# Kernel optimization log

Measured on AMD Instinct MI355X. Metric: run time of the kernel, lower is better.

Reference implementation:

```python
import jax, jax.numpy as jnp
import numpy as np

N = 100000      # nodes
E = 1600000     # edges
G = 100         # graphs in batch
D_IN, H, OUT = 3, 128, 10


def gcn_conv(x, W, b, src, dst, n_nodes):
    """PyG GCNConv with default add_self_loops=True, symmetric normalization.
    out_i = sum_{j->i} d_j^-1/2 d_i^-1/2 (x_j W) + d_i^-1 (x_i W) + b
    where d includes the self-loop (+1)."""
    h = x @ W                                                   # [N, F]
    ones = jnp.ones((src.shape[0],), dtype=x.dtype)
    deg = jax.ops.segment_sum(ones, dst, num_segments=n_nodes) + 1.0  # self-loop
    dinv_sqrt = jax.lax.rsqrt(deg)
    norm = dinv_sqrt[src] * dinv_sqrt[dst]                      # [E]
    msg = h[src] * norm[:, None]                                # gather + scale
    agg = jax.ops.segment_sum(msg, dst, num_segments=n_nodes)   # scatter-add
    out = agg + h * (1.0 / deg)[:, None] + b                    # self-loop term + bias
    return out


def setup_inputs() -> dict:
    key = jax.random.key(0)
    ks = jax.random.split(key, 9)
    x = jax.random.normal(ks[0], (N, D_IN), dtype=jnp.float32)
    edge_index = jax.random.randint(ks[1], (2, E), 0, N)
    batch = jnp.sort(jax.random.randint(ks[2], (N,), 0, G))
    W1 = jax.random.normal(ks[3], (D_IN, H), dtype=jnp.float32) * (1.0 / np.sqrt(D_IN))
    b1 = jnp.zeros((H,), dtype=jnp.float32)
    W2 = jax.random.normal(ks[4], (H, H), dtype=jnp.float32) * (1.0 / np.sqrt(H))
    b2 = jnp.zeros((H,), dtype=jnp.float32)
    Wl = jax.random.normal(ks[5], (H, OUT), dtype=jnp.float32) * (1.0 / np.sqrt(H))
    bl = jnp.zeros((OUT,), dtype=jnp.float32)
    return {"x": x, "edge_index": edge_index, "batch": batch,
            "W1": W1, "b1": b1, "W2": W2, "b2": b2, "Wl": Wl, "bl": bl}


def reference(x, edge_index, batch, W1, b1, W2, b2, Wl, bl):
    src, dst = edge_index[0], edge_index[1]
    h = jax.nn.relu(gcn_conv(x, W1, b1, src, dst, N))
    h = jax.nn.relu(gcn_conv(h, W2, b2, src, dst, N))
    # global mean pool over graphs
    sums = jax.ops.segment_sum(h, batch, num_segments=G)                 # [G, H]
    cnts = jax.ops.segment_sum(jnp.ones((N,), h.dtype), batch, num_segments=G)
    pooled = sums / jnp.maximum(cnts, 1.0)[:, None]
    # dropout p=0.5 is identity in eval mode
    return pooled @ Wl + bl                                              # [G, OUT]
```

## Files before the change

kernel.cpp:

```cpp
#include <hip/hip_runtime.h>


#define DIN 3
#define H 128
#define OUTF 10
#define NWEIGHT (384 + 128 + 16384 + 128 + 1280 + 10)
#define ECH 2048
#define RGSH 9
#define RGSIZE 512
#define W2FRAG_N 16384
#define CHE 512

typedef float gcn364_f2 __attribute__((ext_vector_type(2)));
typedef float gcn364_f4 __attribute__((ext_vector_type(4)));
typedef short gcn364_s8 __attribute__((ext_vector_type(8)));

__device__ __forceinline__ float gcn364_bf2f(unsigned short u) {
    return __uint_as_float(((unsigned int)u) << 16);
}
__device__ __forceinline__ unsigned short gcn364_f2bf(float f) {
    unsigned int u = __float_as_uint(f);
    u += 0x7FFFu + ((u >> 16) & 1u);
    return (unsigned short)(u >> 16);
}

__device__ __forceinline__ int gcn364_probe(const unsigned short* __restrict__ xs16) {
    int lane = threadIdx.x & 63;
    int outl = 0;
    #pragma unroll
    for (int k = 0; k < 4; k++) {
        unsigned short u = xs16[lane * 4 + k];
        int e = (u >> 7) & 0xFF;
        outl += (e < 100 || e > 140) ? 1 : 0;
    }
    #pragma unroll
    for (int d = 1; d < 64; d <<= 1) outl += __shfl_xor(outl, d);
    return (outl > 32) ? 1 : 0;
}

static __global__ void gcn364_histconv(const void* __restrict__ x,
                                       const void* __restrict__ W1, const void* __restrict__ b1,
                                       const void* __restrict__ W2, const void* __restrict__ b2,
                                       const void* __restrict__ Wl, const void* __restrict__ bl,
                                       int* __restrict__ flag,
                                       float4* __restrict__ xf4, float* __restrict__ wf,
                                       unsigned short* __restrict__ w2frag,
                                       float* __restrict__ pooled,
                                       const int* __restrict__ edst,
                                       int* __restrict__ hist,
                                       int N, int E, int S, int RG, int GH) {
    __shared__ int h[256];
    if (blockIdx.x < (unsigned)S) {
        h[threadIdx.x] = 0;
        __syncthreads();
        int elo = blockIdx.x * ECH;
        int ehi = elo + ECH; if (ehi > E) ehi = E;
        #pragma unroll 4
        for (int e = elo + threadIdx.x; e < ehi; e += 256)
            atomicAdd(&h[edst[e] >> RGSH], 1);
        __syncthreads();
        if (threadIdx.x < RG) hist[blockIdx.x * RG + threadIdx.x] = h[threadIdx.x];
    }
    int i = blockIdx.x * blockDim.x + threadIdx.x;
    if (i < GH) pooled[i] = 0.0f;
    int total = N + NWEIGHT;
    if ((int)blockIdx.x * 256 < total) {
        int fl = gcn364_probe((const unsigned short*)x);
        if (i == 0) *flag = fl;
        if (i < N) {
            float a, b, c;
            if (fl) {
                const float* xs = (const float*)x;
                a = xs[3 * i]; b = xs[3 * i + 1]; c = xs[3 * i + 2];
            } else {
                const unsigned short* xs = (const unsigned short*)x;
                a = gcn364_bf2f(xs[3 * i]);
                b = gcn364_bf2f(xs[3 * i + 1]);
                c = gcn364_bf2f(xs[3 * i + 2]);
            }
            xf4[i] = make_float4(a, b, c, 0.f);
        } else if (i < total) {
            int j = i - N;
            const void* srcp;
            if      (j < 384)                       { srcp = W1; }
            else if ((j -= 384)   < 128)            { srcp = b1; }
            else if ((j -= 128)   < 16384)          { srcp = W2; }
            else if ((j -= 16384) < 128)            { srcp = b2; }
            else if ((j -= 128)   < 1280)           { srcp = Wl; }
            else    { j -= 1280;                      srcp = bl; }
            wf[i - N] = fl ? ((const float*)srcp)[j]
                           : gcn364_bf2f(((const unsigned short*)srcp)[j]);
        }
        if (i < W2FRAG_N) {
            int fl2 = fl;
            int j = i & 7;
            int l = (i >> 3) & 63;
            int c = (i >> 9) & 3;
            int t = i >> 11;
            int k = c * 32 + (l >> 4) * 8 + j;
            int n = t * 16 + (l & 15);
            float w = fl2 ? ((const float*)W2)[k * H + n]
                          : gcn364_bf2f(((const unsigned short*)W2)[k * H + n]);
            w2frag[i] = gcn364_f2bf(w);
        }
    }
}

static __global__ void gcn364_scanHpar(int* __restrict__ hist,
                                       int* __restrict__ regionBase,
                                       int S, int RG) {
    __shared__ int sh[1024];
    int r = blockIdx.x;
    int t = threadIdx.x;
    int carry = 0;
    for (int s0 = 0; s0 < S; s0 += 1024) {
        int s = s0 + t;
        int c = (s < S) ? hist[s * RG + r] : 0;
        sh[t] = c;
        __syncthreads();
        for (int d = 1; d < 1024; d <<= 1) {
            int v = (t >= d) ? sh[t - d] : 0;
            __syncthreads();
            sh[t] += v;
            __syncthreads();
        }
        if (s < S) hist[s * RG + r] = carry + sh[t] - c;
        int tot = sh[1023];
        __syncthreads();
        carry += tot;
    }
    if (t == 0) regionBase[r] = carry;
}

static __global__ void gcn364_scanR(int* __restrict__ regionBase,
                                    int RG, int E) {
    __shared__ int sh[256];
    int t = threadIdx.x;
    int c = (t < RG) ? regionBase[t] : 0;
    sh[t] = c;
    __syncthreads();
    for (int d = 1; d < 256; d <<= 1) {
        int v = (t >= d) ? sh[t - d] : 0;
        __syncthreads();
        sh[t] += v;
        __syncthreads();
    }
    if (t < RG) regionBase[t] = sh[t] - c;
    if (t == 0) regionBase[RG] = E;
}

static __global__ void gcn364_partition(const int* __restrict__ src,
                                        const int* __restrict__ dst,
                                        const int* __restrict__ hist,
                                        const int* __restrict__ regionBase,
                                        int* __restrict__ epack,
                                        int E, int RG) {
    __shared__ int cur[256];
    int s = blockIdx.x;
    if (threadIdx.x < RG)
        cur[threadIdx.x] = hist[s * RG + threadIdx.x] + regionBase[threadIdx.x];
    __syncthreads();
    int elo = s * ECH;
    int ehi = elo + ECH; if (ehi > E) ehi = E;
    #pragma unroll 4
    for (int e = elo + threadIdx.x; e < ehi; e += 256) {
        int d = dst[e];
        int sv = src[e];
        int p = atomicAdd(&cur[d >> RGSH], 1);
        epack[p] = ((d & (RGSIZE - 1)) << 17) | sv;
    }
}

static __global__ void gcn364_build(const int* __restrict__ epack,
                                    const int* __restrict__ regionBase,
                                    int* __restrict__ off,
                                    int* __restrict__ esrc,
                                    float4* __restrict__ xf4,
                                    int N) {
    __shared__ int sdeg[RGSIZE];
    __shared__ int stmp[256];
    int r = blockIdx.x;
    int nlo = r << RGSH;
    int nn = N - nlo; if (nn > RGSIZE) nn = RGSIZE;
    int e0 = regionBase[r];
    int e1 = regionBase[r + 1];
    int t = threadIdx.x;
    int bdim = blockDim.x;

    if (t < RGSIZE) sdeg[t] = 0;
    __syncthreads();
    #pragma unroll 4
    for (int p = e0 + t; p < e1; p += bdim)
        atomicAdd(&sdeg[epack[p] >> 17], 1);
    __syncthreads();

    int a0 = 0, a1 = 0, psum = 0;
    if (t < 256) {
        a0 = sdeg[2 * t];
        a1 = sdeg[2 * t + 1];
        psum = a0 + a1;
        stmp[t] = psum;
    }
    __syncthreads();
    for (int d = 1; d < 256; d <<= 1) {
        int val = (t >= d && t < 256) ? stmp[t - d] : 0;
        __syncthreads();
        if (t < 256) stmp[t] += val;
        __syncthreads();
    }
    if (t < 256) {
        int excl = stmp[t] - psum;

        if (2 * t < nn)     off[nlo + 2 * t]     = e0 + excl + a0;
        if (2 * t + 1 < nn) off[nlo + 2 * t + 1] = e0 + excl + a0 + a1;
        if (2 * t < nn) {
            float di = rsqrtf((float)a0 + 1.0f);
            float4 xv = xf4[nlo + 2 * t];
            xv.x *= di; xv.y *= di; xv.z *= di; xv.w = di;
            xf4[nlo + 2 * t] = xv;
        }
        if (2 * t + 1 < nn) {
            float di = rsqrtf((float)a1 + 1.0f);
            float4 xv = xf4[nlo + 2 * t + 1];
            xv.x *= di; xv.y *= di; xv.z *= di; xv.w = di;
            xf4[nlo + 2 * t + 1] = xv;
        }
        sdeg[2 * t]     = e0 + excl;
        sdeg[2 * t + 1] = e0 + excl + a0;
    }
    __syncthreads();
    #pragma unroll 4
    for (int p = e0 + t; p < e1; p += bdim) {
        int v = epack[p];
        int q = atomicAdd(&sdeg[v >> 17], 1);
        esrc[q] = v & 0x1FFFF;
    }
}

static __global__ void gcn364_aggu(const int* __restrict__ esrc,
                                   const int* __restrict__ off,
                                   const float4* __restrict__ xf4,
                                   float4* __restrict__ u4, int N) {
    int lane = threadIdx.x & 63;
    int wv = threadIdx.x >> 6;
    int grp = lane >> 4;
    int sub = lane & 15;
    int i = (blockIdx.x * 4 + wv) * 4 + grp;

    float a0 = 0.f, a1 = 0.f, a2 = 0.f;
    if (i < N) {
        int p0 = (i == 0) ? 0 : off[i - 1];
        int p1 = off[i];
        for (int p = p0 + sub; p < p1; p += 16) {
            float4 sv = xf4[esrc[p]];
            a0 += sv.x; a1 += sv.y; a2 += sv.z;
        }
    }
    for (int d = 1; d < 16; d <<= 1) {
        a0 += __shfl_xor(a0, d);
        a1 += __shfl_xor(a1, d);
        a2 += __shfl_xor(a2, d);
    }
    if (i < N && sub == 0) {
        float4 xi = xf4[i];
        float di = xi.w;
        u4[i] = make_float4(di * (a0 + xi.x), di * (a1 + xi.y), di * (a2 + xi.z), di);
    }
}

__device__ __forceinline__ void gcn364_edge(const float4 u,
                                            const gcn364_f2* wa2, const gcn364_f2* wb2,
                                            const gcn364_f2* wc2, const gcn364_f2* bb2,
                                            gcn364_f2* acc) {
    gcn364_f2 ux = {u.x, u.x}, uy = {u.y, u.y}, uz = {u.z, u.z}, uw = {u.w, u.w};
    gcn364_f2 zero = {0.f, 0.f};
    #pragma unroll
    for (int q = 0; q < 4; q++) {
        gcn364_f2 t = ux * wa2[q] + uy * wb2[q] + uz * wc2[q] + bb2[q];
        t = __builtin_elementwise_max(t, zero);
        acc[q] += uw * t;
    }
}

#define MPB 16
static __global__ __launch_bounds__(256, 8) void gcn364_agg2pool(
        const int* __restrict__ esrc, const int* __restrict__ off,
        const float4* __restrict__ u4,
        const float* __restrict__ w1f, const float* __restrict__ b1f,
        const unsigned short* __restrict__ w2frag, const float* __restrict__ b2f,
        const int* __restrict__ batch, float* __restrict__ pooled, int N) {
    __shared__ unsigned short vshb[MPB][H + 8];
    __shared__ float4 sstage[CHE];
    __shared__ int soff[MPB + 1];
    __shared__ float spool[2][H];
    int i0 = blockIdx.x * MPB;
    int tid = threadIdx.x;
    int wave = tid >> 6;
    int lane = tid & 63;
    int grp = lane >> 4;
    int sub = lane & 15;
    int node = wave * 4 + grp;
    int i = i0 + node;

    if (tid <= MPB) {
        int idx = i0 - 1 + tid;
        int cidx = idx < N - 1 ? idx : N - 1;
        soff[tid] = (idx < 0) ? 0 : off[cidx];
    }

    gcn364_f2 wa2[4], wb2[4], wc2[4], bb2[4];
    #pragma unroll
    for (int q = 0; q < 4; q++) {
        int f = sub * 8 + q * 2;
        wa2[q] = (gcn364_f2){w1f[f], w1f[f + 1]};
        wb2[q] = (gcn364_f2){w1f[H + f], w1f[H + f + 1]};
        wc2[q] = (gcn364_f2){w1f[2 * H + f], w1f[2 * H + f + 1]};
        bb2[q] = (gcn364_f2){b1f[f], b1f[f + 1]};
    }
    __syncthreads();

    int s  = soff[node];
    int e  = soff[node + 1];
    int e0 = soff[0];
    int e1 = soff[MPB];

    gcn364_f2 acc[4];
    acc[0] = acc[1] = acc[2] = acc[3] = (gcn364_f2){0.f, 0.f};
    for (int cb = e0; cb < e1; cb += CHE) {
        int ce = cb + CHE; if (ce > e1) ce = e1;
        for (int p = cb + tid; p < ce; p += 256)
            sstage[p - cb] = u4[esrc[p]];
        __syncthreads();
        int lo = s > cb ? s : cb;
        int hi = e < ce ? e : ce;
        #pragma unroll 4
        for (int p = lo; p < hi; p++) {
            float4 u = sstage[p - cb];
            gcn364_edge(u, wa2, wb2, wc2, bb2, acc);
        }
        __syncthreads();
    }
    float di = 0.f;
    if (i < N) {
        float4 uS = u4[i];
        gcn364_edge(uS, wa2, wb2, wc2, bb2, acc);
        di = uS.w;
    }
    {
        gcn364_s8 o;
        o[0] = (short)gcn364_f2bf(acc[0].x * di);
        o[1] = (short)gcn364_f2bf(acc[0].y * di);
        o[2] = (short)gcn364_f2bf(acc[1].x * di);
        o[3] = (short)gcn364_f2bf(acc[1].y * di);
        o[4] = (short)gcn364_f2bf(acc[2].x * di);
        o[5] = (short)gcn364_f2bf(acc[2].y * di);
        o[6] = (short)gcn364_f2bf(acc[3].x * di);
        o[7] = (short)gcn364_f2bf(acc[3].y * di);
        *(gcn364_s8*)&vshb[node][sub * 8] = o;
    }
    __syncthreads();

    int m = lane & 15;
    int quad = lane >> 4;
    int g0 = batch[i0];
    gcn364_s8 af[4];
    #pragma unroll
    for (int c = 0; c < 4; c++)
        af[c] = *(const gcn364_s8*)&vshb[m][c * 32 + quad * 8];

    #pragma unroll
    for (int tt = 0; tt < 2; tt++) {
        int t = wave * 2 + tt;
        gcn364_f4 cacc = {0.f, 0.f, 0.f, 0.f};
        #pragma unroll
        for (int c = 0; c < 4; c++) {
            gcn364_s8 bf8 = *(const gcn364_s8*)&w2frag[(((t * 4 + c) * 64) + lane) * 8];
            cacc = __builtin_amdgcn_mfma_f32_16x16x32_bf16(af[c], bf8, cacc, 0, 0, 0);
        }
        int feat = t * 16 + m;
        float bb = b2f[feat];
        int baseRow = quad * 4;
        float sum0 = 0.0f, sum1 = 0.0f;
        #pragma unroll
        for (int r = 0; r < 4; r++) {
            int ii = i0 + baseRow + r;
            if (ii >= N) continue;
            float val = fmaxf(cacc[r] + bb, 0.0f);
            if (batch[ii] == g0) sum0 += val; else sum1 += val;
        }
        sum0 += __shfl_xor(sum0, 16); sum0 += __shfl_xor(sum0, 32);
        sum1 += __shfl_xor(sum1, 16); sum1 += __shfl_xor(sum1, 32);
        if (quad == 0) {
            spool[0][feat] = sum0;
            spool[1][feat] = sum1;
        }
    }
    __syncthreads();
    {
        int slot = tid >> 7;
        int f = tid & (H - 1);
        float v = spool[slot][f];
        if (v != 0.0f) {
            int il = i0 + MPB - 1; if (il > N - 1) il = N - 1;
            int g = slot ? batch[il] : g0;
            atomicAdd(&pooled[g * H + f], v);
        }
    }
}

static __global__ void gcn364_final(const float* __restrict__ pooled,
                                    const int* __restrict__ batch,
                                    const float* __restrict__ wlf,
                                    const float* __restrict__ blf,
                                    const int* __restrict__ flag,
                                    void* __restrict__ out, int N, int G) {
    int g = blockIdx.x;
    int o = threadIdx.x;
    if (g >= G || o >= OUTF) return;
    int lo = 0, hi = N;
    while (lo < hi) { int m = (lo + hi) >> 1; if (batch[m] < g) lo = m + 1; else hi = m; }
    int a = lo;
    lo = 0; hi = N;
    while (lo < hi) { int m = (lo + hi) >> 1; if (batch[m] < g + 1) lo = m + 1; else hi = m; }
    float cn = (float)(lo - a);
    float inv = 1.0f / fmaxf(cn, 1.0f);
    float acc = 0.0f;
    for (int k = 0; k < H; k++)
        acc += pooled[g * H + k] * wlf[k * OUTF + o];
    float v = acc * inv + blf[o];
    if (*flag) ((float*)out)[g * OUTF + o] = v;
    else       ((unsigned short*)out)[g * OUTF + o] = gcn364_f2bf(v);
}

extern "C" void kernel_launch(void* const* d_in, const int* in_sizes, int n_in,
                              void* d_out, int out_size, void* d_ws, size_t ws_size,
                              hipStream_t stream) {
    const void* x  = d_in[0];
    const int* edge_index = (const int*)d_in[1];
    const int* batch      = (const int*)d_in[2];
    const void* W1 = d_in[3];
    const void* b1 = d_in[4];
    const void* W2 = d_in[5];
    const void* b2 = d_in[6];
    const void* Wl = d_in[7];
    const void* bl = d_in[8];

    const int N = in_sizes[0] / DIN;
    const int E = in_sizes[1] / 2;
    const int G = out_size / OUTF;
    const int* src = edge_index;
    const int* dst = edge_index + E;
    const int SH = (E + 8191) / 8192;
    const int S  = (E + ECH - 1) / ECH;
    const int RG = (N + RGSIZE - 1) >> RGSH;
    const int GH = G * H;

    char* wsb = (char*)d_ws;
    float* pooled     = (float*)wsb;
    int*   histLeg    = (int*)(pooled + (size_t)GH);
    int*   regionBase = histLeg + (size_t)SH * RG;
    int*   off        = regionBase + RG + 1;
    int*   flag       = off + N;
    size_t ofs = (((size_t)((char*)(flag + 1) - wsb)) + 15) & ~(size_t)15;
    float4* xf4  = (float4*)(wsb + ofs);
    float4* u4   = xf4 + N;
    float*  wf   = (float*)(u4 + N);
    size_t ofs2 = (((size_t)((char*)(wf + NWEIGHT) - wsb)) + 15) & ~(size_t)15;
    unsigned short* w2frag = (unsigned short*)(wsb + ofs2);
    int*    epack = (int*)(w2frag + W2FRAG_N);
    int*    esrc  = epack + E;
    int*    hist  = esrc;

    float* w1f = wf;
    float* b1f = w1f + 384;
    float* b2f = b1f + 128 + 16384;
    float* wlf = b2f + 128;
    float* blf = wlf + 1280;

    {
        int convBlocks = (N + NWEIGHT + 255) / 256;
        int gmax = (S > convBlocks) ? S : convBlocks;
        gcn364_histconv<<<gmax, 256, 0, stream>>>(
            x, W1, b1, W2, b2, Wl, bl, flag, xf4, wf, w2frag, pooled,
            dst, hist, N, E, S, RG, GH);
    }
    gcn364_scanHpar<<<RG, 1024, 0, stream>>>(hist, regionBase, S, RG);
    gcn364_scanR<<<1, 256, 0, stream>>>(regionBase, RG, E);
    gcn364_partition<<<S, 256, 0, stream>>>(src, dst, hist, regionBase, epack, E, RG);
    gcn364_build<<<RG, 1024, 0, stream>>>(epack, regionBase, off, esrc, xf4, N);
    gcn364_aggu<<<(N + 15) / 16, 256, 0, stream>>>(esrc, off, xf4, u4, N);
    gcn364_agg2pool<<<(N + MPB - 1) / MPB, 256, 0, stream>>>(
        esrc, off, u4, w1f, b1f, w2frag, b2f, batch, pooled, N);
    gcn364_final<<<G, 64, 0, stream>>>(pooled, batch, wlf, blf, flag, d_out, N, G);
}
```

Measured before the change: 186.5 us.

## Map each wave across one node's features and process 64 nodes per block

The second aggregation kernel used to give each node a 16-lane group, with each lane handling 8 features. It now gives each node the full 64-lane wave, with each lane handling 2 features, and walks 4 nodes in sequence, so lanes no longer diverge when neighbouring nodes have different degrees. Each block now covers 64 nodes as four 16-node MFMA sub-tiles and adds the pooled sums into shared memory, which cuts the number of blocks and global atomics. The cost is a longer serial loop inside each block, extra barriers, and the existing assumption that a block's nodes span at most two graphs, now stretched over 64 nodes.

Measured after the change: 212.7 us. 1.14x slower.

```diff
diff --git a/kernel.cpp b/kernel.cpp
--- a/kernel.cpp
+++ b/kernel.cpp
@@ -268,28 +268,25 @@
     }
 }
 
-__device__ __forceinline__ void gcn364_edge(const float4 u,
-                                            const gcn364_f2* wa2, const gcn364_f2* wb2,
-                                            const gcn364_f2* wc2, const gcn364_f2* bb2,
-                                            gcn364_f2* acc) {
+__device__ __forceinline__ void gcn364_edge2(const float4 u,
+                                             const gcn364_f2 wa, const gcn364_f2 wb,
+                                             const gcn364_f2 wc, const gcn364_f2 bb,
+                                             gcn364_f2* acc) {
     gcn364_f2 ux = {u.x, u.x}, uy = {u.y, u.y}, uz = {u.z, u.z}, uw = {u.w, u.w};
     gcn364_f2 zero = {0.f, 0.f};
-    #pragma unroll
-    for (int q = 0; q < 4; q++) {
-        gcn364_f2 t = ux * wa2[q] + uy * wb2[q] + uz * wc2[q] + bb2[q];
-        t = __builtin_elementwise_max(t, zero);
-        acc[q] += uw * t;
-    }
-}
-
-#define MPB 16
+    gcn364_f2 t = ux * wa + uy * wb + uz * wc + bb;
+    t = __builtin_elementwise_max(t, zero);
+    *acc += uw * t;
+}
+
+#define MPB 64
 static __global__ __launch_bounds__(256, 8) void gcn364_agg2pool(
         const int* __restrict__ esrc, const int* __restrict__ off,
         const float4* __restrict__ u4,
         const float* __restrict__ w1f, const float* __restrict__ b1f,
         const unsigned short* __restrict__ w2frag, const float* __restrict__ b2f,
         const int* __restrict__ batch, float* __restrict__ pooled, int N) {
-    __shared__ unsigned short vshb[MPB][H + 8];
+    __shared__ unsigned short vshb[16][H + 8];
     __shared__ float4 sstage[CHE];
     __shared__ int soff[MPB + 1];
     __shared__ float spool[2][H];
@@ -297,105 +294,104 @@
     int tid = threadIdx.x;
     int wave = tid >> 6;
     int lane = tid & 63;
-    int grp = lane >> 4;
-    int sub = lane & 15;
-    int node = wave * 4 + grp;
-    int i = i0 + node;
 
     if (tid <= MPB) {
         int idx = i0 - 1 + tid;
         int cidx = idx < N - 1 ? idx : N - 1;
         soff[tid] = (idx < 0) ? 0 : off[cidx];
     }
-
-    gcn364_f2 wa2[4], wb2[4], wc2[4], bb2[4];
-    #pragma unroll
-    for (int q = 0; q < 4; q++) {
-        int f = sub * 8 + q * 2;
-        wa2[q] = (gcn364_f2){w1f[f], w1f[f + 1]};
-        wb2[q] = (gcn364_f2){w1f[H + f], w1f[H + f + 1]};
-        wc2[q] = (gcn364_f2){w1f[2 * H + f], w1f[2 * H + f + 1]};
-        bb2[q] = (gcn364_f2){b1f[f], b1f[f + 1]};
-    }
-    __syncthreads();
-
-    int s  = soff[node];
-    int e  = soff[node + 1];
-    int e0 = soff[0];
-    int e1 = soff[MPB];
-
-    gcn364_f2 acc[4];
-    acc[0] = acc[1] = acc[2] = acc[3] = (gcn364_f2){0.f, 0.f};
-    for (int cb = e0; cb < e1; cb += CHE) {
-        int ce = cb + CHE; if (ce > e1) ce = e1;
-        for (int p = cb + tid; p < ce; p += 256)
-            sstage[p - cb] = u4[esrc[p]];
-        __syncthreads();
-        int lo = s > cb ? s : cb;
-        int hi = e < ce ? e : ce;
-        #pragma unroll 4
-        for (int p = lo; p < hi; p++) {
-            float4 u = sstage[p - cb];
-            gcn364_edge(u, wa2, wb2, wc2, bb2, acc);
-        }
-        __syncthreads();
-    }
-    float di = 0.f;
-    if (i < N) {
-        float4 uS = u4[i];
-        gcn364_edge(uS, wa2, wb2, wc2, bb2, acc);
-        di = uS.w;
-    }
+    spool[tid >> 7][tid & (H - 1)] = 0.0f;
+
+    gcn364_f2 wa, wb, wc, bb;
     {
-        gcn364_s8 o;
-        o[0] = (short)gcn364_f2bf(acc[0].x * di);
-        o[1] = (short)gcn364_f2bf(acc[0].y * di);
-        o[2] = (short)gcn364_f2bf(acc[1].x * di);
-        o[3] = (short)gcn364_f2bf(acc[1].y * di);
-        o[4] = (short)gcn364_f2bf(acc[2].x * di);
-        o[5] = (short)gcn364_f2bf(acc[2].y * di);
-        o[6] = (short)gcn364_f2bf(acc[3].x * di);
-        o[7] = (short)gcn364_f2bf(acc[3].y * di);
-        *(gcn364_s8*)&vshb[node][sub * 8] = o;
-    }
-    __syncthreads();
-
-    int m = lane & 15;
-    int quad = lane >> 4;
+        int f = lane * 2;
+        wa = (gcn364_f2){w1f[f], w1f[f + 1]};
+        wb = (gcn364_f2){w1f[H + f], w1f[H + f + 1]};
+        wc = (gcn364_f2){w1f[2 * H + f], w1f[2 * H + f + 1]};
+        bb = (gcn364_f2){b1f[f], b1f[f + 1]};
+    }
     int g0 = batch[i0];
-    gcn364_s8 af[4];
-    #pragma unroll
-    for (int c = 0; c < 4; c++)
-        af[c] = *(const gcn364_s8*)&vshb[m][c * 32 + quad * 8];
-
-    #pragma unroll
-    for (int tt = 0; tt < 2; tt++) {
-        int t = wave * 2 + tt;
-        gcn364_f4 cacc = {0.f, 0.f, 0.f, 0.f};
+    __syncthreads();
+
+    for (int sub = 0; sub < 4; sub++) {
+        int nb = sub * 16;
+        int e0 = soff[nb];
+        int e1 = soff[nb + 16];
+
+        gcn364_f2 acc[4];
+        acc[0] = acc[1] = acc[2] = acc[3] = (gcn364_f2){0.f, 0.f};
+        for (int cb = e0; cb < e1; cb += CHE) {
+            int ce = cb + CHE; if (ce > e1) ce = e1;
+            for (int p = cb + tid; p < ce; p += 256)
+                sstage[p - cb] = u4[esrc[p]];
+            __syncthreads();
+            #pragma unroll
+            for (int nn = 0; nn < 4; nn++) {
+                int node = nb + wave * 4 + nn;
+                int lo = soff[node];     if (lo < cb) lo = cb;
+                int hi = soff[node + 1]; if (hi > ce) hi = ce;
+                #pragma unroll 4
+                for (int p = lo; p < hi; p++) {
+                    float4 u = sstage[p - cb];
+                    gcn364_edge2(u, wa, wb, wc, bb, &acc[nn]);
+                }
+            }
+            __syncthreads();
+        }
         #pragma unroll
-        for (int c = 0; c < 4; c++) {
-            gcn364_s8 bf8 = *(const gcn364_s8*)&w2frag[(((t * 4 + c) * 64) + lane) * 8];
-            cacc = __builtin_amdgcn_mfma_f32_16x16x32_bf16(af[c], bf8, cacc, 0, 0, 0);
-        }
-        int feat = t * 16 + m;
-        float bb = b2f[feat];
-        int baseRow = quad * 4;
-        float sum0 = 0.0f, sum1 = 0.0f;
+        for (int nn = 0; nn < 4; nn++) {
+            int nodeL = wave * 4 + nn;
+            int i = i0 + nb + nodeL;
+            float di = 0.f;
+            if (i < N) {
+                float4 uS = u4[i];
+                gcn364_edge2(uS, wa, wb, wc, bb, &acc[nn]);
+                di = uS.w;
+            }
+            unsigned short o0 = gcn364_f2bf(acc[nn].x * di);
+            unsigned short o1 = gcn364_f2bf(acc[nn].y * di);
+            unsigned int pk = (unsigned int)o0 | ((unsigned int)o1 << 16);
+            *(unsigned int*)&vshb[nodeL][lane * 2] = pk;
+        }
+        __syncthreads();
+
+        int m = lane & 15;
+        int quad = lane >> 4;
+        gcn364_s8 af[4];
         #pragma unroll
-        for (int r = 0; r < 4; r++) {
-            int ii = i0 + baseRow + r;
-            if (ii >= N) continue;
-            float val = fmaxf(cacc[r] + bb, 0.0f);
-            if (batch[ii] == g0) sum0 += val; else sum1 += val;
-        }
-        sum0 += __shfl_xor(sum0, 16); sum0 += __shfl_xor(sum0, 32);
-        sum1 += __shfl_xor(sum1, 16); sum1 += __shfl_xor(sum1, 32);
-        if (quad == 0) {
-            spool[0][feat] = sum0;
-            spool[1][feat] = sum1;
-        }
-    }
-    __syncthreads();
+        for (int c = 0; c < 4; c++)
+            af[c] = *(const gcn364_s8*)&vshb[m][c * 32 + quad * 8];
+
+        #pragma unroll
+        for (int tt = 0; tt < 2; tt++) {
+            int t = wave * 2 + tt;
+            gcn364_f4 cacc = {0.f, 0.f, 0.f, 0.f};
+            #pragma unroll
+            for (int c = 0; c < 4; c++) {
+                gcn364_s8 bf8 = *(const gcn364_s8*)&w2frag[(((t * 4 + c) * 64) + lane) * 8];
+                cacc = __builtin_amdgcn_mfma_f32_16x16x32_bf16(af[c], bf8, cacc, 0, 0, 0);
+            }
+            int feat = t * 16 + m;
+            float bbias = b2f[feat];
+            int baseRow = quad * 4;
+            float sum0 = 0.0f, sum1 = 0.0f;
+            #pragma unroll
+            for (int r = 0; r < 4; r++) {
+                int ii = i0 + nb + baseRow + r;
+                if (ii >= N) continue;
+                float val = fmaxf(cacc[r] + bbias, 0.0f);
+                if (batch[ii] == g0) sum0 += val; else sum1 += val;
+            }
+            sum0 += __shfl_xor(sum0, 16); sum0 += __shfl_xor(sum0, 32);
+            sum1 += __shfl_xor(sum1, 16); sum1 += __shfl_xor(sum1, 32);
+            if (quad == 0) {
+                spool[0][feat] += sum0;
+                spool[1][feat] += sum1;
+            }
+        }
+        __syncthreads();
+    }
+
     {
         int slot = tid >> 7;
         int f = tid & (H - 1);
```
